# Kernel optimization log

Hardware: AMD Instinct MI355X
Metric: run time of the kernel (lower is better)

The kernel has to match this reference:

```python
import jax, jax.numpy as jnp
import numpy as np

NUM_CLASSES = 1000
MOMENTUM = 0.9
EPSILON = 1e-6
N = 65536


def setup_inputs() -> dict:
    key = jax.random.key(0)
    k1, k2 = jax.random.split(key)
    logits = jax.random.normal(k1, (N, NUM_CLASSES), dtype=jnp.float32)
    targets = jax.random.randint(k2, (N,), 0, NUM_CLASSES, dtype=jnp.int64)
    grad_mag = jnp.ones((NUM_CLASSES,), dtype=jnp.float32)  # buffer init = ones
    return {"logits": logits, "targets": targets, "grad_mag": grad_mag}


def reference(logits, targets, grad_mag):
    n = logits.shape[0]
    # per-sample cross entropy, reduction='none'
    logp = jax.nn.log_softmax(logits, axis=-1)  # [N, C]
    ce = -jnp.take_along_axis(logp, targets[:, None], axis=-1)[:, 0]  # [N]

    # per-class mean CE via one segment-reduce pass (replaces the Python loop)
    sums = jax.ops.segment_sum(ce, targets, num_segments=NUM_CLASSES)  # [C]
    counts = jax.ops.segment_sum(jnp.ones_like(ce), targets, num_segments=NUM_CLASSES)
    class_mean = jnp.abs(sums / jnp.maximum(counts, 1.0))

    # EMA update only for classes present in the batch (mask.any())
    present = counts > 0
    new_gm = jnp.where(present,
                       MOMENTUM * grad_mag + (1.0 - MOMENTUM) * class_mean,
                       grad_mag)  # [C]

    # inverse-magnitude weights, renormalized to sum to N
    w = 1.0 / (new_gm[targets] + EPSILON)  # [N]
    w = w / jnp.sum(w) * n
    return jnp.mean(w * ce)
```

## Files before the change

kernel.cpp:

```cpp
#include <hip/hip_runtime.h>
#include <math.h>

#define NUM_C   1000
#define MOM     0.9f
#define EPS     1e-6f

__global__ __launch_bounds__(256) void ce_kernel(const float* __restrict__ logits,
                                                 const int*   __restrict__ targets,
                                                 float* __restrict__ ce,
                                                 float* __restrict__ sums,
                                                 float* __restrict__ counts,
                                                 int n) {
    const int wave = threadIdx.x >> 6;
    const int lane = threadIdx.x & 63;
    const int row  = blockIdx.x * 4 + wave;
    if (row >= n) return;

    const float4* rp = reinterpret_cast<const float4*>(logits + (size_t)row * NUM_C);

    float4 v[4];
    float m = -INFINITY;
#pragma unroll
    for (int j = 0; j < 4; ++j) {
        int idx = j * 64 + lane;
        if (idx < 250) {
            v[j] = rp[idx];
            m = fmaxf(m, fmaxf(fmaxf(v[j].x, v[j].y), fmaxf(v[j].z, v[j].w)));
        } else {
            v[j] = make_float4(0.f, 0.f, 0.f, 0.f);
        }
    }
#pragma unroll
    for (int off = 32; off > 0; off >>= 1)
        m = fmaxf(m, __shfl_xor(m, off, 64));

    float s = 0.f;
#pragma unroll
    for (int j = 0; j < 4; ++j) {
        int idx = j * 64 + lane;
        if (idx < 250) {
            s += expf(v[j].x - m);
            s += expf(v[j].y - m);
            s += expf(v[j].z - m);
            s += expf(v[j].w - m);
        }
    }
#pragma unroll
    for (int off = 32; off > 0; off >>= 1)
        s += __shfl_xor(s, off, 64);

    if (lane == 0) {
        int t = targets[row];
        float lt = logits[(size_t)row * NUM_C + t];
        float c = (m + logf(s)) - lt;
        ce[row] = c;
        atomicAdd(&sums[t], c);
        atomicAdd(&counts[t], 1.0f);
    }
}

__global__ void gm_kernel(const float* __restrict__ gm_in,
                          const float* __restrict__ sums,
                          const float* __restrict__ counts,
                          float* __restrict__ new_gm) {
    int c = blockIdx.x * blockDim.x + threadIdx.x;
    if (c < NUM_C) {
        float cnt = counts[c];
        float g = gm_in[c];
        if (cnt > 0.f) {
            float cm = fabsf(sums[c] / fmaxf(cnt, 1.0f));
            g = MOM * g + (1.0f - MOM) * cm;
        }
        new_gm[c] = g;
    }
}

__global__ __launch_bounds__(256) void weight_kernel(const int*   __restrict__ targets,
                                                     const float* __restrict__ ce,
                                                     const float* __restrict__ new_gm,
                                                     float* __restrict__ accum,
                                                     int n) {
    float sw = 0.f, swc = 0.f;
    for (int i = blockIdx.x * blockDim.x + threadIdx.x; i < n;
         i += gridDim.x * blockDim.x) {
        int t = targets[i];
        float w = 1.0f / (new_gm[t] + EPS);
        sw  += w;
        swc += w * ce[i];
    }
#pragma unroll
    for (int off = 32; off > 0; off >>= 1) {
        sw  += __shfl_xor(sw,  off, 64);
        swc += __shfl_xor(swc, off, 64);
    }
    __shared__ float ssw[4], sswc[4];
    const int lane = threadIdx.x & 63;
    const int wave = threadIdx.x >> 6;
    if (lane == 0) { ssw[wave] = sw; sswc[wave] = swc; }
    __syncthreads();
    if (threadIdx.x == 0) {
        float a = 0.f, b = 0.f;
        for (int w2 = 0; w2 < 4; ++w2) { a += ssw[w2]; b += sswc[w2]; }
        atomicAdd(&accum[0], a);
        atomicAdd(&accum[1], b);
    }
}

__global__ void final_kernel(const float* __restrict__ accum, float* __restrict__ out) {
    if (threadIdx.x == 0) out[0] = accum[1] / accum[0];
}

extern "C" void kernel_launch(void* const* d_in, const int* in_sizes, int n_in,
                              void* d_out, int out_size, void* d_ws, size_t ws_size,
                              hipStream_t stream) {
    const float* logits  = (const float*)d_in[0];
    const int*   targets = (const int*)d_in[1];
    const float* gm      = (const float*)d_in[2];
    float* out = (float*)d_out;

    const int n = in_sizes[1];

    char* ws = (char*)d_ws;
    float* ce     = (float*)ws;
    float* sums   = (float*)(ws + (size_t)n * 4);
    float* counts = sums + NUM_C;
    float* new_gm = counts + NUM_C;
    float* accum  = new_gm + NUM_C;

    hipMemsetAsync(sums, 0, (3 * NUM_C + 2) * sizeof(float), stream);

    ce_kernel<<<(n + 3) / 4, 256, 0, stream>>>(logits, targets, ce, sums, counts, n);
    gm_kernel<<<(NUM_C + 255) / 256, 256, 0, stream>>>(gm, sums, counts, new_gm);
    weight_kernel<<<256, 256, 0, stream>>>(targets, ce, new_gm, accum, n);
    final_kernel<<<1, 64, 0, stream>>>(accum, out);
}
```

Before: 65.85 us.

## Fold weighted mean into per-class sums and merge tail kernels into one

Each sample's weight depends only on its class, so the weighted sums become per-class terms (count*w and sum*w). That removes the per-sample ce buffer and the pass over N in weight_kernel, and one 1024-thread kernel replaces the gm, weight and final kernels. The target logit is taken from registers already loaded rather than by a second global read, and expf/logf become the fast intrinsics. This drops two launches and a memset region, at the cost of some precision from the fast math and a different summation order.

New measurement: 52.84 us. 1.25x faster.

```diff
diff --git a/kernel.cpp b/kernel.cpp
--- a/kernel.cpp
+++ b/kernel.cpp
@@ -7,7 +7,6 @@
 
 __global__ __launch_bounds__(256) void ce_kernel(const float* __restrict__ logits,
                                                  const int*   __restrict__ targets,
-                                                 float* __restrict__ ce,
                                                  float* __restrict__ sums,
                                                  float* __restrict__ counts,
                                                  int n) {
@@ -15,6 +14,10 @@
     const int lane = threadIdx.x & 63;
     const int row  = blockIdx.x * 4 + wave;
     if (row >= n) return;
+
+    const int t  = targets[row];
+    const int tq = t >> 2;
+    const int tc = t & 3;
 
     const float4* rp = reinterpret_cast<const float4*>(logits + (size_t)row * NUM_C);
 
@@ -26,8 +29,6 @@
         if (idx < 250) {
             v[j] = rp[idx];
             m = fmaxf(m, fmaxf(fmaxf(v[j].x, v[j].y), fmaxf(v[j].z, v[j].w)));
-        } else {
-            v[j] = make_float4(0.f, 0.f, 0.f, 0.f);
         }
     }
 #pragma unroll
@@ -35,79 +36,68 @@
         m = fmaxf(m, __shfl_xor(m, off, 64));
 
     float s = 0.f;
+    float lt = 0.f;
 #pragma unroll
     for (int j = 0; j < 4; ++j) {
         int idx = j * 64 + lane;
         if (idx < 250) {
-            s += expf(v[j].x - m);
-            s += expf(v[j].y - m);
-            s += expf(v[j].z - m);
-            s += expf(v[j].w - m);
+            s += __expf(v[j].x - m);
+            s += __expf(v[j].y - m);
+            s += __expf(v[j].z - m);
+            s += __expf(v[j].w - m);
+            if (idx == tq) {
+                float c = (tc == 0) ? v[j].x : (tc == 1) ? v[j].y
+                        : (tc == 2) ? v[j].z : v[j].w;
+                lt = c;
+            }
         }
     }
 #pragma unroll
-    for (int off = 32; off > 0; off >>= 1)
-        s += __shfl_xor(s, off, 64);
+    for (int off = 32; off > 0; off >>= 1) {
+        s  += __shfl_xor(s,  off, 64);
+        lt += __shfl_xor(lt, off, 64);
+    }
 
     if (lane == 0) {
-        int t = targets[row];
-        float lt = logits[(size_t)row * NUM_C + t];
-        float c = (m + logf(s)) - lt;
-        ce[row] = c;
-        atomicAdd(&sums[t], c);
+        float ce = (m + __logf(s)) - lt;
+        atomicAdd(&sums[t], ce);
         atomicAdd(&counts[t], 1.0f);
     }
 }
 
-__global__ void gm_kernel(const float* __restrict__ gm_in,
-                          const float* __restrict__ sums,
-                          const float* __restrict__ counts,
-                          float* __restrict__ new_gm) {
-    int c = blockIdx.x * blockDim.x + threadIdx.x;
+__global__ __launch_bounds__(1024) void finalize_kernel(const float* __restrict__ gm_in,
+                                                        const float* __restrict__ sums,
+                                                        const float* __restrict__ counts,
+                                                        float* __restrict__ out) {
+    const int c = threadIdx.x;
+    float a = 0.f, b = 0.f;
     if (c < NUM_C) {
         float cnt = counts[c];
-        float g = gm_in[c];
+        float s   = sums[c];
+        float g   = gm_in[c];
         if (cnt > 0.f) {
-            float cm = fabsf(sums[c] / fmaxf(cnt, 1.0f));
+            float cm = fabsf(s / fmaxf(cnt, 1.0f));
             g = MOM * g + (1.0f - MOM) * cm;
         }
-        new_gm[c] = g;
-    }
-}
-
-__global__ __launch_bounds__(256) void weight_kernel(const int*   __restrict__ targets,
-                                                     const float* __restrict__ ce,
-                                                     const float* __restrict__ new_gm,
-                                                     float* __restrict__ accum,
-                                                     int n) {
-    float sw = 0.f, swc = 0.f;
-    for (int i = blockIdx.x * blockDim.x + threadIdx.x; i < n;
-         i += gridDim.x * blockDim.x) {
-        int t = targets[i];
-        float w = 1.0f / (new_gm[t] + EPS);
-        sw  += w;
-        swc += w * ce[i];
+        float w = 1.0f / (g + EPS);
+        a = cnt * w;
+        b = s * w;
     }
 #pragma unroll
     for (int off = 32; off > 0; off >>= 1) {
-        sw  += __shfl_xor(sw,  off, 64);
-        swc += __shfl_xor(swc, off, 64);
+        a += __shfl_xor(a, off, 64);
+        b += __shfl_xor(b, off, 64);
     }
-    __shared__ float ssw[4], sswc[4];
+    __shared__ float sa[16], sb[16];
     const int lane = threadIdx.x & 63;
-    const int wave = threadIdx.x >> 6;
-    if (lane == 0) { ssw[wave] = sw; sswc[wave] = swc; }
+    const int wv   = threadIdx.x >> 6;
+    if (lane == 0) { sa[wv] = a; sb[wv] = b; }
     __syncthreads();
     if (threadIdx.x == 0) {
-        float a = 0.f, b = 0.f;
-        for (int w2 = 0; w2 < 4; ++w2) { a += ssw[w2]; b += sswc[w2]; }
-        atomicAdd(&accum[0], a);
-        atomicAdd(&accum[1], b);
+        float A = 0.f, B = 0.f;
+        for (int i = 0; i < 16; ++i) { A += sa[i]; B += sb[i]; }
+        out[0] = B / A;
     }
-}
-
-__global__ void final_kernel(const float* __restrict__ accum, float* __restrict__ out) {
-    if (threadIdx.x == 0) out[0] = accum[1] / accum[0];
 }
 
 extern "C" void kernel_launch(void* const* d_in, const int* in_sizes, int n_in,
@@ -120,17 +110,11 @@
 
     const int n = in_sizes[1];
 
-    char* ws = (char*)d_ws;
-    float* ce     = (float*)ws;
-    float* sums   = (float*)(ws + (size_t)n * 4);
+    float* sums   = (float*)d_ws;
     float* counts = sums + NUM_C;
-    float* new_gm = counts + NUM_C;
-    float* accum  = new_gm + NUM_C;
 
-    hipMemsetAsync(sums, 0, (3 * NUM_C + 2) * sizeof(float), stream);
+    hipMemsetAsync(sums, 0, 2 * NUM_C * sizeof(float), stream);
 
-    ce_kernel<<<(n + 3) / 4, 256, 0, stream>>>(logits, targets, ce, sums, counts, n);
-    gm_kernel<<<(NUM_C + 255) / 256, 256, 0, stream>>>(gm, sums, counts, new_gm);
-    weight_kernel<<<256, 256, 0, stream>>>(targets, ce, new_gm, accum, n);
-    final_kernel<<<1, 64, 0, stream>>>(accum, out);
+    ce_kernel<<<(n + 3) / 4, 256, 0, stream>>>(logits, targets, sums, counts, n);
+    finalize_kernel<<<1, 1024, 0, stream>>>(gm, sums, counts, out);
 }
```
